# Performance work log

Hardware: AMD Instinct MI355X
Metric: run time of the kernel (lower is better)

The kernel has to match this reference:

```python
import jax, jax.numpy as jnp
import numpy as np

EPS_BN = 1e-5
EPS_COS = 1e-8
M_BINS = 10


def _bn(x, g, b):
    # eval-mode BatchNorm2d with running_mean=0, running_var=1
    s = g / jnp.sqrt(1.0 + EPS_BN)
    return x * s[None, :, None, None] + b[None, :, None, None]


def _dw(x, w, pad, dil):
    # depthwise conv, x [B,C,H,W], w [C,1,kh,kw]
    return jax.lax.conv_general_dilated(
        x, w, window_strides=(1, 1), padding=pad, rhs_dilation=dil,
        dimension_numbers=('NCHW', 'OIHW', 'NCHW'),
        feature_group_count=x.shape[1])


def setup_inputs() -> dict:
    key = jax.random.key(0)
    ks = jax.random.split(key, 20)
    B, INP, OUP, H, W = 16, 64, 64, 128, 128
    f32 = jnp.float32
    d = {}
    d['x'] = jax.random.normal(ks[0], (B, INP, H, W), f32)
    d['w_conv1'] = jax.random.normal(ks[1], (OUP, INP), f32) * 0.05
    d['pr_w1'] = jax.random.normal(ks[2], (OUP, 1, 1, 5), f32) * 0.2
    d['pr_w2'] = jax.random.normal(ks[3], (OUP, 1, 5, 1), f32) * 0.2
    d['pr_w3'] = jax.random.normal(ks[4], (OUP, 1, 1, 5), f32) * 0.2
    d['pr_w4'] = jax.random.normal(ks[5], (OUP, 1, 5, 1), f32) * 0.2
    d['pr_gamma'] = 1.0 + 0.1 * jax.random.normal(ks[6], (5, OUP), f32)
    d['pr_beta'] = 0.1 * jax.random.normal(ks[7], (5, OUP), f32)
    d['bn1_g'] = 1.0 + 0.1 * jax.random.normal(ks[8], (OUP,), f32)
    d['bn1_b'] = 0.1 * jax.random.normal(ks[9], (OUP,), f32)
    d['bn2_g'] = 1.0 + 0.1 * jax.random.normal(ks[10], (OUP,), f32)
    d['bn2_b'] = 0.1 * jax.random.normal(ks[11], (OUP,), f32)
    d['fc1_w'] = jax.random.normal(ks[12], (OUP, 2), f32) * 0.5
    d['fc1_b'] = 0.1 * jax.random.normal(ks[13], (OUP,), f32)
    d['phi1_w'] = jax.random.normal(ks[14], (OUP, OUP), f32) * 0.1
    d['phi1_b'] = 0.01 * jax.random.normal(ks[15], (OUP,), f32)
    d['phi2_w'] = jax.random.normal(ks[16], (OUP, OUP), f32) * 0.1
    d['phi2_b'] = 0.01 * jax.random.normal(ks[17], (OUP,), f32)
    d['phi3_w'] = jax.random.normal(ks[18], (OUP, OUP), f32) * 0.1
    d['phi3_b'] = 0.01 * jax.random.normal(ks[19], (OUP,), f32)
    d['w_conv2'] = jax.random.normal(jax.random.fold_in(key, 99), (OUP, 1), f32) * 0.1
    return d


def reference(x, w_conv1, pr_w1, pr_w2, pr_w3, pr_w4, pr_gamma, pr_beta,
              bn1_g, bn1_b, bn2_g, bn2_b, fc1_w, fc1_b,
              phi1_w, phi1_b, phi2_w, phi2_b, phi3_w, phi3_b, w_conv2):
    B, C, H, W = x.shape
    M = M_BINS
    OUP = w_conv1.shape[0]
    # conv1 (1x1) + Position_reinforcement branch
    x_c = jnp.einsum('oc,bchw->bohw', w_conv1, x)
    h = _bn(x_c, pr_gamma[0], pr_beta[0])
    h = _dw(h, pr_w1, ((0, 0), (2, 2)), (1, 1))
    h = _bn(h, pr_gamma[1], pr_beta[1])
    h = _dw(h, pr_w2, ((2, 2), (0, 0)), (1, 1))
    h = _bn(h, pr_gamma[2], pr_beta[2])
    h = _dw(h, pr_w3, ((0, 0), (4, 4)), (2, 2))
    h = _bn(h, pr_gamma[3], pr_beta[3])
    h = _dw(h, pr_w4, ((4, 4), (0, 0)), (2, 2))
    x_center = _bn(h, pr_gamma[4], pr_beta[4])
    # cosine similarity of each pixel feature with the global-avg feature
    g = jnp.mean(x, axis=(2, 3), keepdims=True)             # [B,C,1,1]
    num = jnp.sum(g * x, axis=1)                            # [B,H,W]
    gn = jnp.maximum(jnp.sqrt(jnp.sum(g * g, axis=1)), EPS_COS)
    xn = jnp.maximum(jnp.sqrt(jnp.sum(x * x, axis=1)), EPS_COS)
    S = num / (gn * xn)                                     # [B,H,W]
    Sf = S.reshape(B, H * W)
    # torch casts min/max with float() -> detached constants
    mn = jax.lax.stop_gradient(jnp.min(Sf, axis=1))
    mx = jax.lax.stop_gradient(jnp.max(Sf, axis=1))
    t = jnp.arange(M, dtype=x.dtype) / (M - 1)
    levels = mn[:, None] + (mx - mn)[:, None] * t[None, :]  # [B,M]
    diff = jnp.abs(levels[:, None, :] - Sf[:, :, None])     # [B,HW,M] soft bins
    V = jnp.where(diff < 0.5 / M, 1.0 - diff, jnp.zeros((), x.dtype))
    colsum = jnp.sum(V, axis=1)                             # [B,M]
    # torch normalizes by V.sum() while only columns 0..j are filled -> cumsum
    denom = jnp.cumsum(colsum, axis=1)
    Ch = jnp.stack([colsum / denom, levels], axis=-1)       # [B,M,2]
    Cf = Ch.reshape(-1, 2) @ fc1_w.T + fc1_b                # [B*M,OUP]
    Cq = Cf.reshape(B, OUP, M)                              # raw view as in torch
    p1 = jnp.einsum('oc,bcm->bom', phi1_w, Cq) + phi1_b[None, :, None]
    p2 = jnp.einsum('oc,bcm->bom', phi2_w, Cq) + phi2_b[None, :, None]
    X = jax.nn.softmax(jnp.einsum('bcm,bcn->bmn', p1, p2), axis=-1)  # [B,M,M]
    p3 = jnp.einsum('oc,bcm->bom', phi3_w, Cq) + phi3_b[None, :, None]
    Lp = jnp.einsum('bcm,bmn->bcn', p3, X)                  # [B,OUP,M]
    Vr = V.reshape(B, M, H * W)                             # raw view as in torch
    R = jnp.einsum('bcm,bmk->bck', Lp, Vr).reshape(B, OUP, H, W)
    x_tex = _bn(R, bn1_g, bn1_b)
    x_full = _bn(w_conv2[:, 0][None, :, None, None] * S[:, None, :, :], bn2_g, bn2_b)
    att = jax.nn.sigmoid(x_full + x_tex + x_center)
    return x * att
```

## Files before the change

kernel.cpp:

```cpp
#include <hip/hip_runtime.h>
#include <hip/hip_bf16.h>
#include <math.h>

#define NB   16
#define NC   64
#define NH   128
#define NW   128
#define NHW  16384
#define NM   10

__global__ __launch_bounds__(256) void k_gmean(const float* __restrict__ x,
                                               double* __restrict__ g) {
    int bc = blockIdx.x;
    const float* xp = x + (size_t)bc * NHW;
    double s = 0.0;
    for (int i = threadIdx.x; i < NHW / 4; i += 256) {
        float4 v = ((const float4*)xp)[i];
        s += (double)v.x + (double)v.y + (double)v.z + (double)v.w;
    }
    for (int off = 32; off; off >>= 1) s += __shfl_down(s, off);
    __shared__ double red[4];
    int wid = threadIdx.x >> 6, lane = threadIdx.x & 63;
    if (lane == 0) red[wid] = s;
    __syncthreads();
    if (threadIdx.x == 0)
        g[bc] = (red[0] + red[1] + red[2] + red[3]) * (1.0 / (double)NHW);
}

__global__ __launch_bounds__(512) void k_conv1_S(
        const float* __restrict__ x, const float* __restrict__ W,
        const double* __restrict__ g, float* __restrict__ xc,
        double* __restrict__ S) {
    __shared__ __align__(16) float Xs[64 * 256];
    __shared__ __align__(16) float Wt[64 * 64];
    int bid = blockIdx.x;
    int b = bid >> 6, k0 = (bid & 63) * 256;
    int tid = threadIdx.x;
    const float* xb = x + (size_t)b * NC * NHW + k0;

    for (int e = tid; e < 64 * 64; e += 512) {
        int c = e >> 6, o = e & 63;
        Wt[c * 64 + o] = W[o * 64 + c];
    }
    for (int e = tid; e < 64 * 64; e += 512) {
        int c = e >> 6, p4 = (e & 63) << 2;
        *(float4*)&Xs[c * 256 + p4] =
            *(const float4*)&xb[(size_t)c * NHW + p4];
    }
    __syncthreads();

    if (tid < 256) {
        const double* gb = g + b * NC;
        double num = 0.0, sq = 0.0, gsq = 0.0;
#pragma unroll
        for (int c = 0; c < NC; ++c) {
            double v = (double)Xs[c * 256 + tid];
            double gc = gb[c];
            num += gc * v;
            sq  += v * v;
            gsq += gc * gc;
        }
        double gn = fmax(sqrt(gsq), 1e-8);
        double xn = fmax(sqrt(sq), 1e-8);
        S[(size_t)b * NHW + k0 + tid] = num / (gn * xn);
    }

    int pg = tid & 63, og = tid >> 6;
    int px0 = pg * 4, o0 = og * 8;
    float acc[8][4];
#pragma unroll
    for (int i = 0; i < 8; ++i)
#pragma unroll
        for (int j = 0; j < 4; ++j) acc[i][j] = 0.f;

#pragma unroll 4
    for (int c = 0; c < NC; ++c) {
        float4 xa = *(float4*)&Xs[c * 256 + px0];
        float4 wa = *(float4*)&Wt[c * 64 + o0];
        float4 wb2 = *(float4*)&Wt[c * 64 + o0 + 4];
        float xr[4] = {xa.x, xa.y, xa.z, xa.w};
        float wr[8] = {wa.x, wa.y, wa.z, wa.w, wb2.x, wb2.y, wb2.z, wb2.w};
#pragma unroll
        for (int i = 0; i < 8; ++i)
#pragma unroll
            for (int j = 0; j < 4; ++j)
                acc[i][j] = fmaf(wr[i], xr[j], acc[i][j]);
    }

    float* xcb = xc + (size_t)b * NC * NHW + k0;
#pragma unroll
    for (int i = 0; i < 8; ++i) {
        float4 s0;
        s0.x = acc[i][0]; s0.y = acc[i][1]; s0.z = acc[i][2]; s0.w = acc[i][3];
        *(float4*)&xcb[(size_t)(o0 + i) * NHW + px0] = s0;
    }
}

__global__ __launch_bounds__(256) void k_chain(
        const double* __restrict__ S,
        const float* __restrict__ fc1w, const float* __restrict__ fc1b,
        const float* __restrict__ ph1w, const float* __restrict__ ph1b,
        const float* __restrict__ ph2w, const float* __restrict__ ph2b,
        const float* __restrict__ ph3w, const float* __restrict__ ph3b,
        double* __restrict__ levelsOut, float* __restrict__ LpOut) {
    int b = blockIdx.x, tid = threadIdx.x;
    const double* Sb = S + b * NHW;

    double mn = 1e300, mx = -1e300;
    for (int i = tid; i < NHW; i += 256) {
        double v = Sb[i];
        mn = fmin(mn, v); mx = fmax(mx, v);
    }
    for (int off = 32; off; off >>= 1) {
        mn = fmin(mn, __shfl_down(mn, off));
        mx = fmax(mx, __shfl_down(mx, off));
    }
    __shared__ double rmn[4], rmx[4];
    int wid = tid >> 6, lane = tid & 63;
    if (lane == 0) { rmn[wid] = mn; rmx[wid] = mx; }
    __syncthreads();
    __shared__ double levS[NM];
    if (tid == 0) {
        double a = fmin(fmin(rmn[0], rmn[1]), fmin(rmn[2], rmn[3]));
        double z = fmax(fmax(rmx[0], rmx[1]), fmax(rmx[2], rmx[3]));
        for (int m = 0; m < NM; ++m) levS[m] = a + (z - a) * ((double)m / 9.0);
    }
    __syncthreads();
    double lv[NM];
#pragma unroll
    for (int m = 0; m < NM; ++m) lv[m] = levS[m];

    double bins[NM];
#pragma unroll
    for (int m = 0; m < NM; ++m) bins[m] = 0.0;
    for (int i = tid; i < NHW; i += 256) {
        double v = Sb[i];
#pragma unroll
        for (int m = 0; m < NM; ++m) {
            double d = fabs(lv[m] - v);
            if (d < 0.05) bins[m] += 1.0 - d;
        }
    }
#pragma unroll
    for (int m = 0; m < NM; ++m)
        for (int off = 32; off; off >>= 1) bins[m] += __shfl_down(bins[m], off);
    __shared__ double wb[4][NM];
    if (lane == 0) {
#pragma unroll
        for (int m = 0; m < NM; ++m) wb[wid][m] = bins[m];
    }
    __syncthreads();
    __shared__ float ratio[NM];
    if (tid == 0) {
        double den = 0.0;
        for (int m = 0; m < NM; ++m) {
            double cs = wb[0][m] + wb[1][m] + wb[2][m] + wb[3][m];
            den += cs;
            ratio[m] = (float)(cs / den);
        }
    }
    __syncthreads();

    __shared__ float CfL[640];
    for (int idx = tid; idx < 640; idx += 256) {
        int rm = idx >> 6, o = idx & 63;
        CfL[idx] = ratio[rm] * fc1w[o*2+0] + (float)levS[rm] * fc1w[o*2+1] + fc1b[o];
    }
    __syncthreads();

    __shared__ float P1[640], P2[640], P3[640];
    for (int idx = tid; idx < 640; idx += 256) {
        int o = idx / 10, m = idx - o * 10;
        float a1 = ph1b[o], a2 = ph2b[o], a3 = ph3b[o];
        for (int c2 = 0; c2 < NC; ++c2) {
            float cq = CfL[c2*10 + m];
            a1 = fmaf(ph1w[o*NC + c2], cq, a1);
            a2 = fmaf(ph2w[o*NC + c2], cq, a2);
            a3 = fmaf(ph3w[o*NC + c2], cq, a3);
        }
        P1[idx] = a1; P2[idx] = a2; P3[idx] = a3;
    }
    __syncthreads();

    __shared__ float XL[100];
    if (tid < 100) {
        int m = tid / 10, n = tid - (tid/10)*10;
        float acc = 0.f;
        for (int c2 = 0; c2 < NC; ++c2)
            acc = fmaf(P1[c2*10 + m], P2[c2*10 + n], acc);
        XL[tid] = acc;
    }
    __syncthreads();
    if (tid < NM) {
        float mxr = XL[tid*10];
        for (int n = 1; n < NM; ++n) mxr = fmaxf(mxr, XL[tid*10 + n]);
        float e[NM], sum = 0.f;
        for (int n = 0; n < NM; ++n) { e[n] = expf(XL[tid*10+n] - mxr); sum += e[n]; }
        for (int n = 0; n < NM; ++n) XL[tid*10+n] = e[n] / sum;
    }
    __syncthreads();

    for (int idx = tid; idx < 640; idx += 256) {
        int c2 = idx / 10, n = idx - (idx/10)*10;
        float acc = 0.f;
#pragma unroll
        for (int m = 0; m < NM; ++m) acc = fmaf(P3[c2*10 + m], XL[m*10 + n], acc);
        LpOut[b*640 + idx] = acc;
    }
    if (tid < NM) levelsOut[b*NM + tid] = levS[tid];
}

__global__ __launch_bounds__(256) void k_vgath(
        const double* __restrict__ S, const double* __restrict__ levels,
        float* __restrict__ vg, float* __restrict__ Sf) {
    int P = blockIdx.x * 256 + threadIdx.x;
    int b = P >> 14, k = P & (NHW - 1);
    __shared__ double levL[NM];
    if (threadIdx.x < NM) levL[threadIdx.x] = levels[b*NM + threadIdx.x];
    __syncthreads();
    const double* Sb = S + (size_t)b * NHW;
    float* vgb = vg + (size_t)b * NM * NHW;
#pragma unroll
    for (int i = 0; i < NM; ++i) {
        int j = i * NHW + k;
        int p = j / 10;
        int m = j - p * 10;
        double d = fabs(levL[m] - Sb[p]);
        vgb[i * NHW + k] = (d < 0.05) ? (float)(1.0 - d) : 0.f;
    }
    Sf[P] = (float)Sb[k];
}

__global__ __launch_bounds__(256) void k_dwfinal(
        const float* __restrict__ xc, const float* __restrict__ x,
        const float* __restrict__ vg, const float* __restrict__ Sf,
        const float* __restrict__ Lp,
        const float* __restrict__ pw1, const float* __restrict__ pw2,
        const float* __restrict__ pw3, const float* __restrict__ pw4,
        const float* __restrict__ gamma, const float* __restrict__ beta,
        const float* __restrict__ bn1g, const float* __restrict__ bn1b,
        const float* __restrict__ bn2g, const float* __restrict__ bn2b,
        const float* __restrict__ wconv2, float* __restrict__ out) {
    int tile = blockIdx.x, c = blockIdx.y, b = blockIdx.z;
    int R0 = (tile >> 1) * 64, C0 = (tile & 1) * 64;
    const float inv = 0.9999950000374997f;
    float s0 = gamma[0*NC+c]*inv, b0 = beta[0*NC+c];
    float s1 = gamma[1*NC+c]*inv, b1 = beta[1*NC+c];
    float s2 = gamma[2*NC+c]*inv, b2 = beta[2*NC+c];
    float s3 = gamma[3*NC+c]*inv, b3 = beta[3*NC+c];
    float s4 = gamma[4*NC+c]*inv, b4 = beta[4*NC+c];
    float w1[5], w2[5], w3[5], w4[5];
#pragma unroll
    for (int q = 0; q < 5; ++q) {
        w1[q] = pw1[c*5+q]; w2[q] = pw2[c*5+q];
        w3[q] = pw3[c*5+q]; w4[q] = pw4[c*5+q];
    }
    float Ac = wconv2[c] * (bn2g[c] * inv);
    float Bc = bn2b[c] + bn1b[c];
    float S1 = bn1g[c] * inv;

    __shared__ __align__(16) float A[76*76];
    __shared__ __align__(16) float Bf[76*72];
    __shared__ float LpL[NM];
    const float* src = xc + ((size_t)(b*NC + c)) * NHW;
    int tid = threadIdx.x;

    if (tid < NM) LpL[tid] = Lp[b*640 + c*10 + tid];

    for (int t = tid; t < 76*19; t += 256) {
        int r = t / 19, g2 = t - r*19;
        int gy = R0 - 6 + r, gx0 = C0 - 6 + 4*g2;
        float4 v = make_float4(0.f, 0.f, 0.f, 0.f);
        bool rowOK = (unsigned)gy < NH;
        if (rowOK) {
            const float* rowp = src + gy*NW;
            if ((unsigned)gx0 <= (unsigned)(NW-4)) {
                v = *(const float4*)(rowp + gx0);
            } else {
                float* pv = (float*)&v;
#pragma unroll
                for (int u = 0; u < 4; ++u) {
                    int gx = gx0 + u;
                    if ((unsigned)gx < NW) pv[u] = rowp[gx];
                }
            }
        }
        float4 w;
        w.x = (rowOK && (unsigned)(gx0+0) < NW) ? fmaf(v.x, s0, b0) : 0.f;
        w.y = (rowOK && (unsigned)(gx0+1) < NW) ? fmaf(v.y, s0, b0) : 0.f;
        w.z = (rowOK && (unsigned)(gx0+2) < NW) ? fmaf(v.z, s0, b0) : 0.f;
        w.w = (rowOK && (unsigned)(gx0+3) < NW) ? fmaf(v.w, s0, b0) : 0.f;
        *(float4*)&A[r*76 + 4*g2] = w;
    }
    __syncthreads();

    for (int t = tid; t < 76*18; t += 256) {
        int r = t / 18, g2 = t - r*18;
        float xw[8];
        *(float4*)&xw[0] = *(float4*)&A[r*76 + 4*g2];
        *(float4*)&xw[4] = *(float4*)&A[r*76 + 4*g2 + 4];
        int gy = R0 - 6 + r;
        bool rowOK = (unsigned)gy < NH;
        float o[4];
#pragma unroll
        for (int u = 0; u < 4; ++u) {
            float acc = 0.f;
#pragma unroll
            for (int q = 0; q < 5; ++q) acc = fmaf(w1[q], xw[u+q], acc);
            int gx = C0 - 4 + 4*g2 + u;
            o[u] = (rowOK && (unsigned)gx < NW) ? fmaf(acc, s1, b1) : 0.f;
        }
        *(float4*)&Bf[r*72 + 4*g2] = *(float4*)o;
    }
    __syncthreads();

    for (int t = tid; t < 72*18; t += 256) {
        int r = t / 18, g2 = t - r*18;
        float ys[5][4];
#pragma unroll
        for (int p = 0; p < 5; ++p)
            *(float4*)&ys[p][0] = *(float4*)&Bf[(r+p)*72 + 4*g2];
        int gy = R0 - 4 + r;
        bool rowOK = (unsigned)gy < NH;
        float o[4];
#pragma unroll
        for (int u = 0; u < 4; ++u) {
            float acc = 0.f;
#pragma unroll
            for (int p = 0; p < 5; ++p) acc = fmaf(w2[p], ys[p][u], acc);
            int gx = C0 - 4 + 4*g2 + u;
            o[u] = (rowOK && (unsigned)gx < NW) ? fmaf(acc, s2, b2) : 0.f;
        }
        *(float4*)&A[r*72 + 4*g2] = *(float4*)o;
    }
    __syncthreads();

    for (int t = tid; t < 72*16; t += 256) {
        int r = t >> 4, g2 = t & 15;
        float xw[12];
        *(float4*)&xw[0] = *(float4*)&A[r*72 + 4*g2];
        *(float4*)&xw[4] = *(float4*)&A[r*72 + 4*g2 + 4];
        *(float4*)&xw[8] = *(float4*)&A[r*72 + 4*g2 + 8];
        int gy = R0 - 4 + r;
        bool rowOK = (unsigned)gy < NH;
        float o[4];
#pragma unroll
        for (int u = 0; u < 4; ++u) {
            float acc = 0.f;
#pragma unroll
            for (int q = 0; q < 5; ++q) acc = fmaf(w3[q], xw[u+2*q], acc);
            o[u] = rowOK ? fmaf(acc, s3, b3) : 0.f;
        }
        *(float4*)&Bf[r*64 + 4*g2] = *(float4*)o;
    }
    __syncthreads();

    const float* vgb = vg + (size_t)b * NM * NHW;
    const float* Sfb = Sf + (size_t)b * NHW;
    for (int t = tid; t < 64*16; t += 256) {
        int r = t >> 4, g2 = t & 15;
        float ys[5][4];
#pragma unroll
        for (int p = 0; p < 5; ++p)
            *(float4*)&ys[p][0] = *(float4*)&Bf[(r+2*p)*64 + 4*g2];
        int kbase = (R0 + r) * NW + C0 + 4*g2;
        size_t xbase = (size_t)(b*NC + c) * NHW + kbase;
        float4 xv = *(const float4*)&x[xbase];
        float4 skv = *(const float4*)&Sfb[kbase];
        const float* xvp = (const float*)&xv;
        const float* skp = (const float*)&skv;
        float vr[NM][4];
#pragma unroll
        for (int i = 0; i < NM; ++i)
            *(float4*)&vr[i][0] = *(const float4*)&vgb[i * NHW + kbase];
        float res[4];
#pragma unroll
        for (int u = 0; u < 4; ++u) {
            float acc = 0.f;
#pragma unroll
            for (int p = 0; p < 5; ++p) acc = fmaf(w4[p], ys[p][u], acc);
            float xcen = fmaf(acc, s4, b4);
            float R = 0.f;
#pragma unroll
            for (int i = 0; i < NM; ++i) R = fmaf(LpL[i], vr[i][u], R);
            float pre = fmaf(Ac, skp[u], Bc) + S1 * R + xcen;
            float att = 1.0f / (1.0f + expf(-pre));
            res[u] = xvp[u] * att;
        }
        *(float4*)&out[xbase] = *(float4*)res;
    }
}

extern "C" void kernel_launch(void* const* d_in, const int* in_sizes, int n_in,
                              void* d_out, int out_size, void* d_ws, size_t ws_size,
                              hipStream_t stream) {
    (void)in_sizes; (void)n_in; (void)out_size; (void)ws_size;
    const float* x      = (const float*)d_in[0];
    const float* wconv1 = (const float*)d_in[1];
    const float* pw1    = (const float*)d_in[2];
    const float* pw2    = (const float*)d_in[3];
    const float* pw3    = (const float*)d_in[4];
    const float* pw4    = (const float*)d_in[5];
    const float* pgam   = (const float*)d_in[6];
    const float* pbet   = (const float*)d_in[7];
    const float* bn1g   = (const float*)d_in[8];
    const float* bn1b   = (const float*)d_in[9];
    const float* bn2g   = (const float*)d_in[10];
    const float* bn2b   = (const float*)d_in[11];
    const float* fc1w   = (const float*)d_in[12];
    const float* fc1b   = (const float*)d_in[13];
    const float* ph1w   = (const float*)d_in[14];
    const float* ph1b   = (const float*)d_in[15];
    const float* ph2w   = (const float*)d_in[16];
    const float* ph2b   = (const float*)d_in[17];
    const float* ph3w   = (const float*)d_in[18];
    const float* ph3b   = (const float*)d_in[19];
    const float* wconv2 = (const float*)d_in[20];
    float* out = (float*)d_out;

    float*  ws  = (float*)d_ws;
    float*  xc  = ws;
    double* Sd  = (double*)(ws + 16777216);
    double* g   = Sd + NB * NHW;
    double* lev = g + NB * NC;
    float*  Lp  = (float*)(lev + NB * NM);
    float*  vg  = Lp + NB * 640;
    float*  Sf  = vg + NB * NM * NHW;

    k_gmean<<<NB * NC, 256, 0, stream>>>(x, g);
    k_conv1_S<<<NB * NHW / 256, 512, 0, stream>>>(x, wconv1, g, xc, Sd);
    k_chain<<<NB, 256, 0, stream>>>(Sd, fc1w, fc1b, ph1w, ph1b, ph2w, ph2b,
                                    ph3w, ph3b, lev, Lp);
    k_vgath<<<NB * NHW / 256, 256, 0, stream>>>(Sd, lev, vg, Sf);
    k_dwfinal<<<dim3(4, NC, NB), 256, 0, stream>>>(
        xc, x, vg, Sf, Lp, pw1, pw2, pw3, pw4, pgam, pbet,
        bn1g, bn1b, bn2g, bn2b, wconv2, out);
}
```

Measured before the change: 189.8 us.

## Precompute transposed conv1 weights and gnorm, shrink dwfinal row tiles

A new small kernel transposes the 1x1 conv weights and computes the per-batch global-mean norm once, so each conv1 block no longer rebuilds them. The conv1 kernel reads weights from global memory at a wave-uniform offset (readfirstlane), which lets them be scalar loads and frees LDS. The depthwise/final kernel halves its row tile to 32 rows and doubles its grid, cutting LDS per block and raising occupancy, at the cost of more halo recomputation and reload. It also adds one extra kernel launch.

```diff
diff --git a/kernel.cpp b/kernel.cpp
--- a/kernel.cpp
+++ b/kernel.cpp
@@ -27,22 +27,35 @@
         g[bc] = (red[0] + red[1] + red[2] + red[3]) * (1.0 / (double)NHW);
 }
 
+__global__ __launch_bounds__(256) void k_misc(const float* __restrict__ W,
+                                              const double* __restrict__ g,
+                                              float* __restrict__ Wt,
+                                              double* __restrict__ gn) {
+    if (blockIdx.x == 0) {
+        for (int e = threadIdx.x; e < 64 * 64; e += 256) {
+            int c = e >> 6, o = e & 63;
+            Wt[c * 64 + o] = W[o * 64 + c];
+        }
+    } else if (threadIdx.x == 0) {
+        int b = blockIdx.x - 1;
+        const double* gb = g + b * NC;
+        double gsq = 0.0;
+        for (int c = 0; c < NC; ++c) gsq += gb[c] * gb[c];
+        gn[b] = fmax(sqrt(gsq), 1e-8);
+    }
+}
+
 __global__ __launch_bounds__(512) void k_conv1_S(
-        const float* __restrict__ x, const float* __restrict__ W,
-        const double* __restrict__ g, float* __restrict__ xc,
-        double* __restrict__ S) {
+        const float* __restrict__ x, const float* __restrict__ Wt,
+        const double* __restrict__ g, const double* __restrict__ gn,
+        float* __restrict__ xc, double* __restrict__ S) {
     __shared__ __align__(16) float Xs[64 * 256];
-    __shared__ __align__(16) float Wt[64 * 64];
     int bid = blockIdx.x;
     int b = bid >> 6, k0 = (bid & 63) * 256;
     int tid = threadIdx.x;
     const float* xb = x + (size_t)b * NC * NHW + k0;
 
     for (int e = tid; e < 64 * 64; e += 512) {
-        int c = e >> 6, o = e & 63;
-        Wt[c * 64 + o] = W[o * 64 + c];
-    }
-    for (int e = tid; e < 64 * 64; e += 512) {
         int c = e >> 6, p4 = (e & 63) << 2;
         *(float4*)&Xs[c * 256 + p4] =
             *(const float4*)&xb[(size_t)c * NHW + p4];
@@ -51,22 +64,19 @@
 
     if (tid < 256) {
         const double* gb = g + b * NC;
-        double num = 0.0, sq = 0.0, gsq = 0.0;
+        double num = 0.0, sq = 0.0;
 #pragma unroll
         for (int c = 0; c < NC; ++c) {
             double v = (double)Xs[c * 256 + tid];
-            double gc = gb[c];
-            num += gc * v;
+            num += gb[c] * v;
             sq  += v * v;
-            gsq += gc * gc;
-        }
-        double gn = fmax(sqrt(gsq), 1e-8);
+        }
         double xn = fmax(sqrt(sq), 1e-8);
-        S[(size_t)b * NHW + k0 + tid] = num / (gn * xn);
-    }
-
-    int pg = tid & 63, og = tid >> 6;
-    int px0 = pg * 4, o0 = og * 8;
+        S[(size_t)b * NHW + k0 + tid] = num / (gn[b] * xn);
+    }
+
+    int o0 = __builtin_amdgcn_readfirstlane((tid >> 6) * 8);
+    int px0 = (tid & 63) * 4;
     float acc[8][4];
 #pragma unroll
     for (int i = 0; i < 8; ++i)
@@ -76,15 +86,16 @@
 #pragma unroll 4
     for (int c = 0; c < NC; ++c) {
         float4 xa = *(float4*)&Xs[c * 256 + px0];
-        float4 wa = *(float4*)&Wt[c * 64 + o0];
-        float4 wb2 = *(float4*)&Wt[c * 64 + o0 + 4];
+        const float* wr = Wt + c * 64 + o0;
         float xr[4] = {xa.x, xa.y, xa.z, xa.w};
-        float wr[8] = {wa.x, wa.y, wa.z, wa.w, wb2.x, wb2.y, wb2.z, wb2.w};
+        float wv[8];
+#pragma unroll
+        for (int i = 0; i < 8; ++i) wv[i] = wr[i];
 #pragma unroll
         for (int i = 0; i < 8; ++i)
 #pragma unroll
             for (int j = 0; j < 4; ++j)
-                acc[i][j] = fmaf(wr[i], xr[j], acc[i][j]);
+                acc[i][j] = fmaf(wv[i], xr[j], acc[i][j]);
     }
 
     float* xcb = xc + (size_t)b * NC * NHW + k0;
@@ -242,7 +253,7 @@
         const float* __restrict__ bn2g, const float* __restrict__ bn2b,
         const float* __restrict__ wconv2, float* __restrict__ out) {
     int tile = blockIdx.x, c = blockIdx.y, b = blockIdx.z;
-    int R0 = (tile >> 1) * 64, C0 = (tile & 1) * 64;
+    int R0 = (tile >> 1) * 32, C0 = (tile & 1) * 64;
     const float inv = 0.9999950000374997f;
     float s0 = gamma[0*NC+c]*inv, b0 = beta[0*NC+c];
     float s1 = gamma[1*NC+c]*inv, b1 = beta[1*NC+c];
@@ -259,15 +270,15 @@
     float Bc = bn2b[c] + bn1b[c];
     float S1 = bn1g[c] * inv;
 
-    __shared__ __align__(16) float A[76*76];
-    __shared__ __align__(16) float Bf[76*72];
+    __shared__ __align__(16) float A[44*76];
+    __shared__ __align__(16) float Bf[44*72];
     __shared__ float LpL[NM];
     const float* src = xc + ((size_t)(b*NC + c)) * NHW;
     int tid = threadIdx.x;
 
     if (tid < NM) LpL[tid] = Lp[b*640 + c*10 + tid];
 
-    for (int t = tid; t < 76*19; t += 256) {
+    for (int t = tid; t < 44*19; t += 256) {
         int r = t / 19, g2 = t - r*19;
         int gy = R0 - 6 + r, gx0 = C0 - 6 + 4*g2;
         float4 v = make_float4(0.f, 0.f, 0.f, 0.f);
@@ -294,7 +305,7 @@
     }
     __syncthreads();
 
-    for (int t = tid; t < 76*18; t += 256) {
+    for (int t = tid; t < 44*18; t += 256) {
         int r = t / 18, g2 = t - r*18;
         float xw[8];
         *(float4*)&xw[0] = *(float4*)&A[r*76 + 4*g2];
@@ -314,7 +325,7 @@
     }
     __syncthreads();
 
-    for (int t = tid; t < 72*18; t += 256) {
+    for (int t = tid; t < 40*18; t += 256) {
         int r = t / 18, g2 = t - r*18;
         float ys[5][4];
 #pragma unroll
@@ -335,7 +346,7 @@
     }
     __syncthreads();
 
-    for (int t = tid; t < 72*16; t += 256) {
+    for (int t = tid; t < 40*16; t += 256) {
         int r = t >> 4, g2 = t & 15;
         float xw[12];
         *(float4*)&xw[0] = *(float4*)&A[r*72 + 4*g2];
@@ -357,7 +368,7 @@
 
     const float* vgb = vg + (size_t)b * NM * NHW;
     const float* Sfb = Sf + (size_t)b * NHW;
-    for (int t = tid; t < 64*16; t += 256) {
+    for (int t = tid; t < 32*16; t += 256) {
         int r = t >> 4, g2 = t & 15;
         float ys[5][4];
 #pragma unroll
@@ -423,16 +434,19 @@
     double* Sd  = (double*)(ws + 16777216);
     double* g   = Sd + NB * NHW;
     double* lev = g + NB * NC;
-    float*  Lp  = (float*)(lev + NB * NM);
+    double* gn  = lev + NB * NM;
+    float*  Lp  = (float*)(gn + NB);
     float*  vg  = Lp + NB * 640;
     float*  Sf  = vg + NB * NM * NHW;
+    float*  Wt  = Sf + NB * NHW;
 
     k_gmean<<<NB * NC, 256, 0, stream>>>(x, g);
-    k_conv1_S<<<NB * NHW / 256, 512, 0, stream>>>(x, wconv1, g, xc, Sd);
+    k_misc<<<17, 256, 0, stream>>>(wconv1, g, Wt, gn);
+    k_conv1_S<<<NB * NHW / 256, 512, 0, stream>>>(x, Wt, g, gn, xc, Sd);
     k_chain<<<NB, 256, 0, stream>>>(Sd, fc1w, fc1b, ph1w, ph1b, ph2w, ph2b,
                                     ph3w, ph3b, lev, Lp);
     k_vgath<<<NB * NHW / 256, 256, 0, stream>>>(Sd, lev, vg, Sf);
-    k_dwfinal<<<dim3(4, NC, NB), 256, 0, stream>>>(
+    k_dwfinal<<<dim3(8, NC, NB), 256, 0, stream>>>(
         xc, x, vg, Sf, Lp, pw1, pw2, pw3, pw4, pgam, pbet,
         bn1g, bn1b, bn2g, bn2b, wconv2, out);
 }
```

After: 170.1 us. 1.12x faster.
